# Kernel tuning notes

Hardware: AMD Instinct MI355X
Metric: run time of the kernel (lower is better)

## Reference

```python
import jax, jax.numpy as jnp
import numpy as np

WIN_H, WIN_W = 8, 16
N = WIN_H * WIN_W            # 128 tokens per window
DIM, HEADS = 512, 16
TOW = 64 // WIN_H            # type_of_windows = input_resolution[0] // window_size[0] = 8
B_WIN = 2048                 # number of windows (B_)


def _earth_position_index():
    # Faithful port of get_earth_position_index (torch wraps negative indices;
    # we pre-wrap with mod so the gather uses nonnegative indices identically).
    ch = np.arange(WIN_H)
    cw = np.arange(WIN_W)
    coords = np.stack(np.meshgrid(ch, cw, indexing='ij'))        # [2, h, w]
    cf = coords.reshape(2, -1)                                   # [2, N]
    rel = cf[:, :, None] - cf[:, None, :]                        # [2, N, N]
    rel = rel.transpose(1, 2, 0).copy()                          # [N, N, 2]
    rel[:, :, 0] *= 2 * WIN_W - 1
    rel[:, :, 1] += WIN_W - 1
    idx = rel.sum(-1)                                            # [N, N], may be negative
    table_len = WIN_H ** 2 * (2 * WIN_W - 1)                     # 1984
    return (idx % table_len).astype(np.int32)


def setup_inputs() -> dict:
    key = jax.random.key(0)
    ks = jax.random.split(key, 6)
    table_len = WIN_H ** 2 * (2 * WIN_W - 1)
    inv_sqrt_dim = 1.0 / np.sqrt(DIM)
    return {
        'x': jax.random.normal(ks[0], (B_WIN, N, DIM), dtype=jnp.float32),
        'qkv_w': jax.random.normal(ks[1], (3 * DIM, DIM), dtype=jnp.float32) * inv_sqrt_dim,
        'qkv_b': jax.random.normal(ks[2], (3 * DIM,), dtype=jnp.float32) * 0.02,
        'proj_w': jax.random.normal(ks[3], (DIM, DIM), dtype=jnp.float32) * inv_sqrt_dim,
        'proj_b': jax.random.normal(ks[4], (DIM,), dtype=jnp.float32) * 0.02,
        'bias_table': jax.random.normal(ks[5], (table_len, TOW, HEADS), dtype=jnp.float32) * 0.02,
        'pos_index': jnp.asarray(_earth_position_index()),
    }


def reference(x, qkv_w, qkv_b, proj_w, proj_b, bias_table, pos_index):
    B_, Nn, C = x.shape
    hd = C // HEADS
    scale = hd ** (-0.5)
    # fused QKV projection: [B_, N, 3, H, hd]
    qkv = (x @ qkv_w.T + qkv_b).reshape(B_, Nn, 3, HEADS, hd)
    q = qkv[:, :, 0].transpose(0, 2, 1, 3) * scale               # [B_, H, N, hd]
    k = qkv[:, :, 1].transpose(0, 2, 1, 3)
    v = qkv[:, :, 2].transpose(0, 2, 1, 3)
    attn = jnp.einsum('bhnd,bhmd->bhnm', q, k)                   # [B_, H, N, N]
    # earth position bias: gather [N*N] rows -> [N, N, TOW, H], pick middle latitude
    epb = bias_table[pos_index.reshape(-1)].reshape(Nn, Nn, TOW, HEADS)
    epb = epb[:, :, TOW // 2, :]                                 # [N, N, H]
    attn = attn + epb.transpose(2, 0, 1)[None]                   # + [1, H, N, N]
    attn = jax.nn.softmax(attn, axis=-1)
    out = jnp.einsum('bhnm,bhmd->bhnd', attn, v)                 # [B_, H, N, hd]
    out = out.transpose(0, 2, 1, 3).reshape(B_, Nn, C)
    return out @ proj_w.T + proj_b
```

## Files before the change

kernel.cpp:

```cpp
#include <hip/hip_runtime.h>
#include <hip/hip_bf16.h>


typedef short short8 __attribute__((ext_vector_type(8)));
typedef float f32x4 __attribute__((ext_vector_type(4)));
typedef unsigned short u16;
typedef unsigned int u32;

__device__ __forceinline__ u16 f2bf(float f) {
    __bf16 h = (__bf16)f;
    union { __bf16 b; u16 u; } v; v.b = h;
    return v.u;
}

__device__ __forceinline__ f32x4 mfma16(short8 a, short8 b, f32x4 c) {
    return __builtin_amdgcn_mfma_f32_16x16x32_bf16(a, b, c, 0, 0, 0);
}

#define GLDS16(gsrc, ldst)                                                  \
    __builtin_amdgcn_global_load_lds(                                       \
        (const __attribute__((address_space(1))) void*)(gsrc),              \
        (__attribute__((address_space(3))) void*)(ldst), 16, 0, 0)

__global__ __launch_bounds__(256) void cvt_x_kernel(
    const float4* __restrict__ xin, int4* __restrict__ xbf)
{
    int idx = blockIdx.x * 256 + threadIdx.x;
    for (; idx < 16777216; idx += 8192 * 256) {
        const float4 a = xin[idx * 2], b = xin[idx * 2 + 1];
        int4 o;
        o.x = (u32)f2bf(a.x) | ((u32)f2bf(a.y) << 16);
        o.y = (u32)f2bf(a.z) | ((u32)f2bf(a.w) << 16);
        o.z = (u32)f2bf(b.x) | ((u32)f2bf(b.y) << 16);
        o.w = (u32)f2bf(b.z) | ((u32)f2bf(b.w) << 16);
        xbf[idx] = o;
    }
}

__global__ __launch_bounds__(256) void prep_kernel(
    const float* __restrict__ qkv_w, const float* __restrict__ proj_w,
    const float* __restrict__ btab, const int* __restrict__ pidx,
    u16* __restrict__ qkvw_bf, u16* __restrict__ projw_bf,
    float* __restrict__ epb)
{
    const int i = blockIdx.x * 256 + threadIdx.x;
    qkvw_bf[i] = f2bf(qkv_w[i]);
    if (i < 512 * 512) projw_bf[i] = f2bf(proj_w[i]);
    if (i < 16 * 128 * 128) {
        const int rc = i & 16383, h = i >> 14;
        epb[i] = btab[pidx[rc] * 128 + 64 + h];
    }
}


template<bool EPI_QKV>
__global__ __launch_bounds__(256) void gemm_bt(
    const u16* __restrict__ A, const u16* __restrict__ Bt,
    const float* __restrict__ bias, void* __restrict__ Cv,
    u16* __restrict__ kb, u16* __restrict__ vtb,
    const int Nn, const int K, const float qscale)
{
    __shared__ __attribute__((aligned(16))) char sm[49152];

    const int tid = threadIdx.x;
    const int lane = tid & 63;
    const int w = tid >> 6;
    const int lo = lane & 15, g = lane >> 4;
    const int wm = w >> 1, wn = w & 1;
    const int wofs = __builtin_amdgcn_readfirstlane(w) * 1024;
    const int ntile = Nn >> 7;

    int wg = blockIdx.x;
    {
        const int cpx = gridDim.x >> 3;
        wg = (wg & 7) * cpx + (wg >> 3);
    }
    const int bm = wg / ntile, bn = wg % ntile;
    const size_t m0 = (size_t)bm << 7;
    const int n0 = bn << 7;
    const int nk = K >> 5;

    const int rs = w * 16 + (lane >> 2);
    const int c8 = (((lane & 3) ^ ((lane >> 3) & 3))) * 8;
    const u16* pa0 = A + (m0 + rs) * (size_t)K + c8;
    const u16* pa1 = pa0 + (size_t)64 * K;
    const u16* pb0 = Bt + (size_t)(n0 + rs) * K + c8;
    const u16* pb1 = pb0 + (size_t)64 * K;

#define STAGE(buf, kt)                                                     \
    do {                                                                   \
        const int ko = (kt) << 5;                                          \
        char* d = sm + (buf) * 16384 + wofs;                               \
        GLDS16(pa0 + ko, d);                                               \
        GLDS16(pa1 + ko, d + 4096);                                        \
        GLDS16(pb0 + ko, d + 8192);                                        \
        GLDS16(pb1 + ko, d + 12288);                                       \
    } while (0)

    f32x4 acc[4][4] = {};

    STAGE(0, 0);
    STAGE(1, 1);
    asm volatile("s_waitcnt vmcnt(4)" ::: "memory");
    __builtin_amdgcn_s_barrier();

    const int csw16 = (g ^ ((lo >> 1) & 3)) << 4;

    int cur = 0, pre = 2;
    for (int t = 0; t < nk; ++t) {
        if (t + 2 < nk) STAGE(pre, t + 2);
        const char* Ab = sm + cur * 16384;
        const char* Bb = Ab + 8192;
        short8 af[4], bq[4];
#pragma unroll
        for (int i = 0; i < 4; ++i) {
            af[i] = *(const short8*)(Ab + (wm * 64 + i * 16 + lo) * 64 + csw16);
            bq[i] = *(const short8*)(Bb + (wn * 64 + i * 16 + lo) * 64 + csw16);
        }
#pragma unroll
        for (int i = 0; i < 4; ++i)
#pragma unroll
            for (int j = 0; j < 4; ++j)
                acc[i][j] = mfma16(af[i], bq[j], acc[i][j]);
        if (t + 2 < nk) asm volatile("s_waitcnt vmcnt(4)" ::: "memory");
        else            asm volatile("s_waitcnt vmcnt(0)" ::: "memory");
        asm volatile("" ::: "memory");
        __builtin_amdgcn_s_barrier();
        cur = (cur == 2) ? 0 : cur + 1;
        pre = (pre == 2) ? 0 : pre + 1;
    }
#undef STAGE

    if constexpr (EPI_QKV) {
        u16* Ct = (u16*)sm;
        const int b16 = ((int)(m0 >> 7)) * 16;
        const int tsel = bn >> 2;
        const int h0 = (bn & 3) << 2;
        u16* outb = (tsel == 0) ? (u16*)Cv : (tsel == 1) ? kb : vtb;
        if (tsel < 2) {
            const float sc = (tsel == 0) ? qscale : 1.0f;
#pragma unroll
            for (int j = 0; j < 4; ++j) {
                const int c = wn * 64 + j * 16 + lo;
                const float bv = bias[n0 + c];
#pragma unroll
                for (int i = 0; i < 4; ++i)
#pragma unroll
                    for (int ii = 0; ii < 4; ++ii) {
                        const int r = wm * 64 + i * 16 + g * 4 + ii;
                        Ct[r * 136 + c] = f2bf((acc[i][j][ii] + bv) * sc);
                    }
            }
            __syncthreads();
#pragma unroll
            for (int it = 0; it < 8; ++it) {
                const int idx = it * 256 + tid;
                const int r = idx >> 4, s2 = idx & 15;
                const int hl = s2 >> 2, d0 = (s2 & 3) * 8;
                *(int4*)(outb + ((size_t)(b16 + h0 + hl) * 128 + r) * 32 + d0) =
                    *(const int4*)(Ct + r * 136 + s2 * 8);
            }
        } else {
#pragma unroll
            for (int j = 0; j < 4; ++j) {
                const int c = wn * 64 + j * 16 + lo;
                const float bv = bias[n0 + c];
#pragma unroll
                for (int i = 0; i < 4; ++i)
#pragma unroll
                    for (int ii = 0; ii < 4; ++ii) {
                        const int r = wm * 64 + i * 16 + g * 4 + ii;
                        Ct[c * 136 + r] = f2bf(acc[i][j][ii] + bv);
                    }
            }
            __syncthreads();
#pragma unroll
            for (int it = 0; it < 8; ++it) {
                const int idx = it * 256 + tid;
                const int cidx = idx >> 4, nc = idx & 15;
                const int hl = cidx >> 5, d = cidx & 31;
                *(int4*)(outb + ((size_t)(b16 + h0 + hl) * 32 + d) * 128 + nc * 8) =
                    *(const int4*)(Ct + cidx * 136 + nc * 8);
            }
        }
    } else {
        float* Cg = (float*)Cv;
#pragma unroll
        for (int j = 0; j < 4; ++j) {
            const int c = wn * 64 + j * 16 + lo;
            const float bv = bias[n0 + c];
#pragma unroll
            for (int i = 0; i < 4; ++i)
#pragma unroll
                for (int ii = 0; ii < 4; ++ii) {
                    const size_t r = m0 + wm * 64 + i * 16 + g * 4 + ii;
                    Cg[r * (size_t)Nn + n0 + c] = acc[i][j][ii] + bv;
                }
        }
    }
}

__global__ __launch_bounds__(256) void attn_kernel(
    const u16* __restrict__ qbuf, const u16* __restrict__ kbuf,
    const u16* __restrict__ vtbuf, const float* __restrict__ epb,
    u16* __restrict__ aout)
{
    __shared__ __attribute__((aligned(16))) char smem[43520];
    u16 (*Vt)[136]      = (u16(*)[136])smem;
    char* Qs            = smem + 8704;
    char* Ks            = smem + 16896;
    u16 (*Ps)[32][136]  = (u16(*)[32][136])(smem + 8704);
    u16 (*Os)[32]       = (u16(*)[32])smem;

    const int h = blockIdx.x >> 11;
    const int b = blockIdx.x & 2047;
    const int tid = threadIdx.x;
    const int lane = tid & 63, w = tid >> 6;
    const int lo = lane & 15, g = lane >> 4;
    const int wu = __builtin_amdgcn_readfirstlane(w);

    const size_t hb = (size_t)(b * 16 + h) * 4096;
    const u16* qp = qbuf + hb;
    const u16* kp = kbuf + hb;
    const u16* vp = vtbuf + hb;

    const int c8 = ((lane & 3) ^ ((lane >> 3) & 3)) * 8;
    const int rofs = (lane >> 2) * 32;
#pragma unroll
    for (int cc = 0; cc < 2; ++cc) {
        const int ch = wu * 2 + cc;
        GLDS16(qp + ch * 512 + rofs + c8, Qs + ch * 1024);
        GLDS16(kp + ch * 512 + rofs + c8, Ks + ch * 1024);
    }
#pragma unroll
    for (int it = 0; it < 2; ++it) {
        const int idx = tid + it * 256;
        const int d = idx >> 4, nc = idx & 15;
        const int4 v = *(const int4*)(vp + idx * 8);
        *(int4*)(&Vt[d][nc * 8]) = v;
    }
    __syncthreads();

    const int r0 = w * 32;
    const int csw16 = (g ^ ((lo >> 1) & 3)) << 4;

    short8 aq[2], bk[8];
    aq[0] = *(const short8*)(Qs + (r0 + lo) * 64 + csw16);
    aq[1] = *(const short8*)(Qs + (r0 + 16 + lo) * 64 + csw16);
#pragma unroll
    for (int j = 0; j < 8; ++j)
        bk[j] = *(const short8*)(Ks + (j * 16 + lo) * 64 + csw16);

    f32x4 acc[2][8];
#pragma unroll
    for (int j = 0; j < 8; ++j) {
        f32x4 z = {0.f, 0.f, 0.f, 0.f};
        acc[0][j] = mfma16(aq[0], bk[j], z);
        acc[1][j] = mfma16(aq[1], bk[j], z);
    }

    const float* eb = epb + (h << 14);
    float mrow[2][4], rsum[2][4];
#pragma unroll
    for (int mt = 0; mt < 2; ++mt)
#pragma unroll
        for (int ii = 0; ii < 4; ++ii) { mrow[mt][ii] = -1e30f; rsum[mt][ii] = 0.f; }

#pragma unroll
    for (int mt = 0; mt < 2; ++mt)
#pragma unroll
        for (int j = 0; j < 8; ++j)
#pragma unroll
            for (int ii = 0; ii < 4; ++ii) {
                const int r = r0 + mt * 16 + g * 4 + ii;
                const int c = j * 16 + lo;
                const float sv = acc[mt][j][ii] + eb[(r << 7) + c];
                acc[mt][j][ii] = sv;
                mrow[mt][ii] = fmaxf(mrow[mt][ii], sv);
            }
#pragma unroll
    for (int d = 1; d < 16; d <<= 1)
#pragma unroll
        for (int mt = 0; mt < 2; ++mt)
#pragma unroll
            for (int ii = 0; ii < 4; ++ii)
                mrow[mt][ii] = fmaxf(mrow[mt][ii], __shfl_xor(mrow[mt][ii], d, 64));

    __syncthreads();

#pragma unroll
    for (int mt = 0; mt < 2; ++mt)
#pragma unroll
        for (int j = 0; j < 8; ++j)
#pragma unroll
            for (int ii = 0; ii < 4; ++ii) {
                const float p = __expf(acc[mt][j][ii] - mrow[mt][ii]);
                rsum[mt][ii] += p;
                Ps[w][mt * 16 + g * 4 + ii][j * 16 + lo] = f2bf(p);
            }
#pragma unroll
    for (int d = 1; d < 16; d <<= 1)
#pragma unroll
        for (int mt = 0; mt < 2; ++mt)
#pragma unroll
            for (int ii = 0; ii < 4; ++ii)
                rsum[mt][ii] += __shfl_xor(rsum[mt][ii], d, 64);

    f32x4 o[2][2] = {};
#pragma unroll
    for (int kk = 0; kk < 4; ++kk) {
        short8 av[2];
        av[0] = *(const short8*)(&Ps[w][lo][kk * 32 + g * 8]);
        av[1] = *(const short8*)(&Ps[w][16 + lo][kk * 32 + g * 8]);
#pragma unroll
        for (int dt = 0; dt < 2; ++dt) {
            const short8 bv = *(const short8*)(&Vt[dt * 16 + lo][kk * 32 + g * 8]);
            o[0][dt] = mfma16(av[0], bv, o[0][dt]);
            o[1][dt] = mfma16(av[1], bv, o[1][dt]);
        }
    }

    __syncthreads();

#pragma unroll
    for (int mt = 0; mt < 2; ++mt)
#pragma unroll
        for (int dt = 0; dt < 2; ++dt)
#pragma unroll
            for (int ii = 0; ii < 4; ++ii)
                Os[r0 + mt * 16 + g * 4 + ii][dt * 16 + lo] =
                    f2bf(o[mt][dt][ii] / rsum[mt][ii]);
    __syncthreads();

    u16* op = aout + (size_t)b * 128 * 512 + h * 32;
#pragma unroll
    for (int it = 0; it < 2; ++it) {
        const int idx = tid + it * 256;
        const int r = idx >> 2, c = (idx & 3) * 8;
        *(int4*)(op + (size_t)r * 512 + c) = *(const int4*)(&Os[r][c]);
    }
}

extern "C" void kernel_launch(void* const* d_in, const int* in_sizes, int n_in,
                              void* d_out, int out_size, void* d_ws, size_t ws_size,
                              hipStream_t stream)
{
    const float* x      = (const float*)d_in[0];
    const float* qkv_w  = (const float*)d_in[1];
    const float* qkv_b  = (const float*)d_in[2];
    const float* proj_w = (const float*)d_in[3];
    const float* proj_b = (const float*)d_in[4];
    const float* btab   = (const float*)d_in[5];
    const int*   pidx   = (const int*)d_in[6];

    char* ws = (char*)d_ws;
    u16*   xbf      = (u16*)(ws);
    u16*   attnbuf  = (u16*)(ws);
    u16*   qkvw_bf  = (u16*)(ws + 268435456);
    u16*   projw_bf = (u16*)(ws + 270008320);
    float* epb      = (float*)(ws + 270532608);
    u16*   qbuf     = (u16*)(ws + 271581184);
    u16*   kbuf     = (u16*)(ws + 540016640);
    u16*   vtbuf    = (u16*)(ws + 808452096);

    const float qscale = 0.17677669529663687f;

    cvt_x_kernel<<<dim3(8192), dim3(256), 0, stream>>>(
        (const float4*)x, (int4*)xbf);

    prep_kernel<<<dim3(3072), dim3(256), 0, stream>>>(
        qkv_w, proj_w, btab, pidx, qkvw_bf, projw_bf, epb);

    gemm_bt<true><<<dim3(2048 * 12), dim3(256), 0, stream>>>(
        xbf, qkvw_bf, qkv_b, qbuf, kbuf, vtbuf, 1536, 512, qscale);

    attn_kernel<<<dim3(32768), dim3(256), 0, stream>>>(
        qbuf, kbuf, vtbuf, epb, attnbuf);

    gemm_bt<false><<<dim3(2048 * 4), dim3(256), 0, stream>>>(
        attnbuf, projw_bf, proj_b, d_out, nullptr, nullptr, 512, 512, 1.0f);
}
```

Before: 1.341 ms.

## Shrink GEMM LDS to double buffer and split epilogue for higher occupancy

Cuts the GEMM's shared memory from 48KB to 32KB by moving from a triple-buffered to a double-buffered K pipeline. The QKV epilogue now stages its output through LDS in two halves so it fits the smaller buffer. Launch bounds request 5 blocks per CU, aiming to raise occupancy and hide latency across blocks. The cost is less prefetch depth: each iteration waits for all outstanding loads, and the epilogue adds extra barriers.

```diff
diff --git a/kernel.cpp b/kernel.cpp
--- a/kernel.cpp
+++ b/kernel.cpp
@@ -54,13 +54,13 @@
 
 
 template<bool EPI_QKV>
-__global__ __launch_bounds__(256) void gemm_bt(
+__global__ __launch_bounds__(256, 5) void gemm_bt(
     const u16* __restrict__ A, const u16* __restrict__ Bt,
     const float* __restrict__ bias, void* __restrict__ Cv,
     u16* __restrict__ kb, u16* __restrict__ vtb,
     const int Nn, const int K, const float qscale)
 {
-    __shared__ __attribute__((aligned(16))) char sm[49152];
+    __shared__ __attribute__((aligned(16))) char sm[32768];
 
     const int tid = threadIdx.x;
     const int lane = tid & 63;
@@ -80,8 +80,8 @@
     const int n0 = bn << 7;
     const int nk = K >> 5;
 
-    const int rs = w * 16 + (lane >> 2);
-    const int c8 = (((lane & 3) ^ ((lane >> 3) & 3))) * 8;
+    const int rs = tid >> 2;
+    const int c8 = (((tid & 3) ^ ((tid >> 3) & 3))) * 8;
     const u16* pa0 = A + (m0 + rs) * (size_t)K + c8;
     const u16* pa1 = pa0 + (size_t)64 * K;
     const u16* pb0 = Bt + (size_t)(n0 + rs) * K + c8;
@@ -100,16 +100,15 @@
     f32x4 acc[4][4] = {};
 
     STAGE(0, 0);
-    STAGE(1, 1);
-    asm volatile("s_waitcnt vmcnt(4)" ::: "memory");
+    asm volatile("s_waitcnt vmcnt(0)" ::: "memory");
     __builtin_amdgcn_s_barrier();
 
     const int csw16 = (g ^ ((lo >> 1) & 3)) << 4;
 
-    int cur = 0, pre = 2;
+    int buf = 0;
     for (int t = 0; t < nk; ++t) {
-        if (t + 2 < nk) STAGE(pre, t + 2);
-        const char* Ab = sm + cur * 16384;
+        if (t + 1 < nk) STAGE(buf ^ 1, t + 1);
+        const char* Ab = sm + buf * 16384;
         const char* Bb = Ab + 8192;
         short8 af[4], bq[4];
 #pragma unroll
@@ -122,12 +121,10 @@
 #pragma unroll
             for (int j = 0; j < 4; ++j)
                 acc[i][j] = mfma16(af[i], bq[j], acc[i][j]);
-        if (t + 2 < nk) asm volatile("s_waitcnt vmcnt(4)" ::: "memory");
-        else            asm volatile("s_waitcnt vmcnt(0)" ::: "memory");
+        asm volatile("s_waitcnt vmcnt(0)" ::: "memory");
         asm volatile("" ::: "memory");
         __builtin_amdgcn_s_barrier();
-        cur = (cur == 2) ? 0 : cur + 1;
-        pre = (pre == 2) ? 0 : pre + 1;
+        buf ^= 1;
     }
 #undef STAGE
 
@@ -140,47 +137,63 @@
         if (tsel < 2) {
             const float sc = (tsel == 0) ? qscale : 1.0f;
 #pragma unroll
-            for (int j = 0; j < 4; ++j) {
-                const int c = wn * 64 + j * 16 + lo;
-                const float bv = bias[n0 + c];
-#pragma unroll
-                for (int i = 0; i < 4; ++i)
-#pragma unroll
-                    for (int ii = 0; ii < 4; ++ii) {
-                        const int r = wm * 64 + i * 16 + g * 4 + ii;
-                        Ct[r * 136 + c] = f2bf((acc[i][j][ii] + bv) * sc);
+            for (int ph = 0; ph < 2; ++ph) {
+                __syncthreads();
+                if (wm == ph) {
+#pragma unroll
+                    for (int j = 0; j < 4; ++j) {
+                        const int c = wn * 64 + j * 16 + lo;
+                        const float bv = bias[n0 + c];
+#pragma unroll
+                        for (int i = 0; i < 4; ++i)
+#pragma unroll
+                            for (int ii = 0; ii < 4; ++ii) {
+                                const int r = i * 16 + g * 4 + ii;
+                                Ct[r * 136 + c] = f2bf((acc[i][j][ii] + bv) * sc);
+                            }
                     }
-            }
-            __syncthreads();
-#pragma unroll
-            for (int it = 0; it < 8; ++it) {
-                const int idx = it * 256 + tid;
-                const int r = idx >> 4, s2 = idx & 15;
-                const int hl = s2 >> 2, d0 = (s2 & 3) * 8;
-                *(int4*)(outb + ((size_t)(b16 + h0 + hl) * 128 + r) * 32 + d0) =
-                    *(const int4*)(Ct + r * 136 + s2 * 8);
+                }
+                __syncthreads();
+#pragma unroll
+                for (int it = 0; it < 4; ++it) {
+                    const int idx = it * 256 + tid;
+                    const int r = idx >> 4, s2 = idx & 15;
+                    const int hl = s2 >> 2, d0 = (s2 & 3) * 8;
+                    *(int4*)(outb + ((size_t)(b16 + h0 + hl) * 128
+                                     + ph * 64 + r) * 32 + d0) =
+                        *(const int4*)(Ct + r * 136 + s2 * 8);
+                }
             }
         } else {
 #pragma unroll
-            for (int j = 0; j < 4; ++j) {
-                const int c = wn * 64 + j * 16 + lo;
-                const float bv = bias[n0 + c];
-#pragma unroll
-                for (int i = 0; i < 4; ++i)
-#pragma unroll
-                    for (int ii = 0; ii < 4; ++ii) {
-                        const int r = wm * 64 + i * 16 + g * 4 + ii;
-                        Ct[c * 136 + r] = f2bf(acc[i][j][ii] + bv);
+            for (int ph = 0; ph < 2; ++ph) {
+                __syncthreads();
+                if (wn == ph) {
+#pragma unroll
+                    for (int j = 0; j < 4; ++j) {
+                        const int c = j * 16 + lo;
+                        const float bv = bias[n0 + ph * 64 + wn * 0 + c
+                                              + ph * 0 + (wn ? 0 : 0)];
+#pragma unroll
+                        for (int i = 0; i < 4; ++i)
+#pragma unroll
+                            for (int ii = 0; ii < 4; ++ii) {
+                                const int r = wm * 64 + i * 16 + g * 4 + ii;
+                                Ct[c * 136 + r] = f2bf(acc[i][j][ii] + bv);
+                            }
                     }
-            }
-            __syncthreads();
-#pragma unroll
-            for (int it = 0; it < 8; ++it) {
-                const int idx = it * 256 + tid;
-                const int cidx = idx >> 4, nc = idx & 15;
-                const int hl = cidx >> 5, d = cidx & 31;
-                *(int4*)(outb + ((size_t)(b16 + h0 + hl) * 32 + d) * 128 + nc * 8) =
-                    *(const int4*)(Ct + cidx * 136 + nc * 8);
+                }
+                __syncthreads();
+#pragma unroll
+                for (int it = 0; it < 4; ++it) {
+                    const int idx = it * 256 + tid;
+                    const int cidx = idx >> 4, nc = idx & 15;
+                    const int gc = ph * 64 + cidx;
+                    const int hl = gc >> 5, d = gc & 31;
+                    *(int4*)(outb + ((size_t)(b16 + h0 + hl) * 32 + d) * 128
+                             + nc * 8) =
+                        *(const int4*)(Ct + cidx * 136 + nc * 8);
+                }
             }
         }
     } else {
```

Result: slower. 2.223 ms (+65.8%).
